# Kernel optimization log

Measured on AMD Instinct MI355X. Metric: run time of the kernel, lower is better.

The kernel has to match this reference:

```python
import jax, jax.numpy as jnp
import numpy as np

B = 16
H, D, DV = 8, 64, 64
MAX_SEQLEN = 1024
ALPHA = 1.0


def setup_inputs() -> dict:
    key = jax.random.key(0)
    lengths = np.array([512 + (b * 97) % 513 for b in range(B)], dtype=np.int32)
    offsets = np.concatenate([[0], np.cumsum(lengths)]).astype(np.int32)  # (B+1,)
    T = int(offsets[-1])  # 12137
    k1, k2, k3 = jax.random.split(key, 3)
    tq = jax.random.normal(k1, (T, H * D), dtype=jnp.float32)
    tk = jax.random.normal(k2, (T, H * D), dtype=jnp.float32)
    tv = jax.random.normal(k3, (T, H * DV), dtype=jnp.float32)
    num_candidates = jnp.full((B,), 32, dtype=jnp.int32)
    num_contextuals = jnp.full((B,), 8, dtype=jnp.int32)
    return {
        "tq": tq, "tk": tk, "tv": tv,
        "offsets": jnp.asarray(offsets),
        "max_seqlen": MAX_SEQLEN,
        "num_candidates": num_candidates,
        "num_contextuals": num_contextuals,
    }


def _valid_attn_mask(N, lengths, num_candidates, num_contextuals):
    # HSTU mask: causal within history, contextual tokens act as position 0
    # (attend/attended bidirectionally w.r.t. history), targets (candidates)
    # attend to all history + themselves only (target_group_size == 1).
    ids = jnp.arange(N, dtype=jnp.int32)[None, :]              # (1, N)
    c = num_contextuals[:, None]                                # (B, 1)
    ids_adj = jnp.maximum(ids - c + 1, 0)                       # (B, N)
    max_ids = (lengths - num_contextuals + 1 - num_candidates)[:, None]  # (B, 1)
    ids_adj = jnp.minimum(ids_adj, max_ids)                     # all targets share id == max_ids
    row = ids_adj[:, :, None]                                   # (B, N, 1)
    col = ids_adj[:, None, :]                                   # (B, 1, N)
    dist = row - col
    eye = jnp.eye(N, dtype=bool)[None]
    valid = eye | (dist > 0)                                    # causal + self
    # contextual rows (adjusted id 0) attend all history (but not targets)
    valid = valid | ((row == 0) & (col < max_ids[:, :, None]))
    # mask out padding
    pad = jnp.arange(N, dtype=jnp.int32)[None, :] < lengths[:, None]  # (B, N)
    valid = valid & pad[:, :, None] & pad[:, None, :]
    return valid


def reference(tq, tk, tv, offsets, max_seqlen, num_candidates, num_contextuals):
    T = tq.shape[0]
    Bb = offsets.shape[0] - 1
    N = max_seqlen
    lengths = offsets[1:] - offsets[:-1]                        # (B,)
    # jagged -> padded dense via scatter
    t = jnp.arange(T, dtype=jnp.int32)
    b_idx = jnp.searchsorted(offsets, t, side="right").astype(jnp.int32) - 1
    n_idx = t - offsets[b_idx]
    q = jnp.zeros((Bb, N, H, D), tq.dtype).at[b_idx, n_idx].set(tq.reshape(T, H, D))
    k = jnp.zeros((Bb, N, H, D), tk.dtype).at[b_idx, n_idx].set(tk.reshape(T, H, D))
    v = jnp.zeros((Bb, N, H, DV), tv.dtype).at[b_idx, n_idx].set(tv.reshape(T, H, DV))
    valid = _valid_attn_mask(N, lengths, num_candidates, num_contextuals)  # (B, N, N)
    qk = jnp.einsum("bnhd,bmhd->bhnm", q, k) * ALPHA
    # HSTU non-softmax attention: silu(scores) / max_seqlen, masked
    attn = (jax.nn.silu(qk) / N) * valid[:, None, :, :].astype(qk.dtype)
    out = jnp.einsum("bhnm,bmhd->bnhd", attn, v)                # (B, N, H, DV)
    # padded -> jagged gather
    return out[b_idx, n_idx].reshape(T, H * DV)
```

## Files before the change

kernel.cpp:

```cpp
#include <hip/hip_runtime.h>
#include <math.h>


#define HH      8
#define DDIM    64
#define QT      64
#define KT      64
#define STRIDE  512
#define NMAX    1024
#define NORD    16
#define TILE_HW 8192
#define NBLK    1024

typedef __attribute__((ext_vector_type(8))) short short8;
typedef __attribute__((ext_vector_type(4))) float f32x4;
typedef __attribute__((ext_vector_type(4))) uint  u32x4;

static __device__ __forceinline__ uint pk2(float a, float b) {
  uint r;
  asm("v_cvt_pk_bf16_f32 %0, %1, %2" : "=v"(r) : "v"(a), "v"(b));
  return r;
}

static __device__ __forceinline__ void dma16(const ushort* g, ushort* l) {
  __builtin_amdgcn_global_load_lds(
      (const __attribute__((address_space(1))) void*)g,
      (__attribute__((address_space(3))) void*)l, 16, 0, 0);
}

__global__ void build_tiles(const float* __restrict__ tk,
                            const float* __restrict__ tv,
                            ushort* __restrict__ tiles,
                            const int* __restrict__ offsets,
                            const int* __restrict__ pN) {
  const int mt = blockIdx.x, h = blockIdx.y, b = blockIdx.z;
  const int off = offsets[b];
  const int L   = offsets[b + 1] - off;
  if (mt * 64 >= L) return;
  const int tid = threadIdx.x;
  const float invN = 1.0f / (float)pN[0];

  __shared__ ushort tr[64][66];

  ushort* img = tiles + (size_t)((b * NORD + mt) * HH + h) * TILE_HW;
  const int row = tid >> 2;
  const int c0  = (tid & 3) * 16;
  const int m   = mt * 64 + row;
  const int sw  = (row & 7) << 3;

  {
    uint u[8];
    if (m < L) {
      const float* s = tk + (size_t)(off + m) * STRIDE + h * DDIM + c0;
      float4 a = *(const float4*)(s),      b4 = *(const float4*)(s + 4);
      float4 c4 = *(const float4*)(s + 8), d4 = *(const float4*)(s + 12);
      u[0] = pk2(a.x, a.y);   u[1] = pk2(a.z, a.w);
      u[2] = pk2(b4.x, b4.y); u[3] = pk2(b4.z, b4.w);
      u[4] = pk2(c4.x, c4.y); u[5] = pk2(c4.z, c4.w);
      u[6] = pk2(d4.x, d4.y); u[7] = pk2(d4.z, d4.w);
    } else {
#pragma unroll
      for (int j = 0; j < 8; ++j) u[j] = 0u;
    }
    *(uint4*)&img[row * 64 + (c0 ^ sw)]       = make_uint4(u[0], u[1], u[2], u[3]);
    *(uint4*)&img[row * 64 + ((c0 + 8) ^ sw)] = make_uint4(u[4], u[5], u[6], u[7]);
  }
  {
    uint u[8];
    if (m < L) {
      const float* s = tv + (size_t)(off + m) * STRIDE + h * DDIM + c0;
      float4 a = *(const float4*)(s),      b4 = *(const float4*)(s + 4);
      float4 c4 = *(const float4*)(s + 8), d4 = *(const float4*)(s + 12);
      u[0] = pk2(a.x * invN, a.y * invN);   u[1] = pk2(a.z * invN, a.w * invN);
      u[2] = pk2(b4.x * invN, b4.y * invN); u[3] = pk2(b4.z * invN, b4.w * invN);
      u[4] = pk2(c4.x * invN, c4.y * invN); u[5] = pk2(c4.z * invN, c4.w * invN);
      u[6] = pk2(d4.x * invN, d4.y * invN); u[7] = pk2(d4.z * invN, d4.w * invN);
    } else {
#pragma unroll
      for (int j = 0; j < 8; ++j) u[j] = 0u;
    }
#pragma unroll
    for (int j = 0; j < 8; ++j) *(uint*)&tr[row][c0 + 2 * j] = u[j];
  }
  __syncthreads();
  {
    const int dv = tid >> 2;
    const int tc = (tid & 3) * 16;
    uint u[8];
#pragma unroll
    for (int j = 0; j < 8; ++j)
      u[j] = (uint)tr[tc + 2 * j][dv] | ((uint)tr[tc + 2 * j + 1][dv] << 16);
    *(uint4*)&img[4096 + row * 64 + (c0 ^ sw)]       = make_uint4(u[0], u[1], u[2], u[3]);
    *(uint4*)&img[4096 + row * 64 + ((c0 + 8) ^ sw)] = make_uint4(u[4], u[5], u[6], u[7]);
  }
}

__global__ void zero_ctr(uint* ctr) { *ctr = 0u; }

__launch_bounds__(256, 4)
__global__ void hstu_s(const float* __restrict__ tq,
                       const ushort* __restrict__ tiles,
                       const int* __restrict__ offsets,
                       const int* __restrict__ ncand,
                       const int* __restrict__ nctx,
                       float* __restrict__ out, int Tm1, int Bb) {
  __shared__ ushort KV[2][TILE_HW];
  __shared__ ushort Ps[4 * 1024];

  const int tid  = threadIdx.x;
  const int w    = tid >> 6;
  const int lane = tid & 63;
  const int lo   = lane & 15;
  const int hi   = lane >> 4;

  int* scr = (int*)Ps;
  if (tid < 16)
    scr[tid] = (tid < Bb) ? (offsets[tid + 1] - offsets[tid] + QT - 1) / QT : 0;
  if (tid >= 16 && tid < 32) scr[tid] = -1;
  __syncthreads();
  if (tid < Bb) {
    const int nqb = scr[tid];
    int r = 0;
#pragma unroll
    for (int j = 0; j < 16; ++j) {
      int v = scr[j];
      r += (j < Bb) & ((v > nqb) | ((v == nqb) & (j < tid)));
    }
    if (r < Bb / 2) scr[16 + (r & 7)] = tid;
    else            scr[24 + ((Bb - 1 - r) & 7)] = tid;
  }
  __syncthreads();
  if (tid == 0) {
    const int g = blockIdx.x & 7, lb = blockIdx.x >> 3;
    const int gb0 = scr[16 + g], gb1 = scr[24 + g];
    const int q0 = (gb0 >= 0) ? scr[gb0] : -1;
    const int q1 = (gb1 >= 0) ? scr[gb1] : -1;
    const int i0 = lb >> 3,         h0 = lb & 7;
    const int i1 = (255 - lb) >> 3, h1 = (255 - lb) & 7;
    int cnt = 0, i = 0, e0 = -1, e1 = -1;
#pragma unroll
    for (int cst = 16; cst >= 1; --cst) {
#pragma unroll
      for (int s = 0; s < 2; ++s) {
        const int bb = (s == 0) ? gb0 : gb1;
        const int q  = (s == 0) ? q0 : q1;
        if (bb < 0) continue;
#pragma unroll
        for (int which = 0; which < 2; ++which) {
          int qt = -1;
          if (which == 0 && cst == q) qt = 0;
          if (which == 1 && cst >= 2 && cst <= q) qt = cst - 1;
          if (qt < 0) continue;
          const int enc = (bb << 7) | qt;
          if (i == i0) { e0 = enc | (h0 << 4); ++cnt; }
          if (i == i1) { e1 = enc | (h1 << 4); ++cnt; }
          ++i;
        }
      }
    }
    if (e0 < 0) { e0 = e1; e1 = -1; }
    scr[32] = e0; scr[33] = e1; scr[34] = cnt;
  }
  __syncthreads();
  const int e0  = scr[32];
  const int e1  = scr[33];
  const int cnt = scr[34];
  if (cnt == 0) return;

  ushort* Pw = &Ps[w * 1024];

  for (int it = 0; it < cnt; ++it) {
    const int e = (it == 0) ? e0 : e1;
    if (e < 0) return;
    const int b = (e >> 7) & 15, h = (e >> 4) & 7, qt = e & 15;
    const int off = offsets[b];
    const int L   = offsets[b + 1] - off;
    const int n0  = qt * QT;
    if (n0 >= L) continue;

    const int c = nctx[b];
    const int M = L - c + 1 - ncand[b];
    const int m_hi  = (n0 < c) ? L : min(n0 + QT, L);
    const int niter = (m_hi + KT - 1) / KT;

    const ushort* ibase = tiles + (size_t)(b * NORD * HH + h) * TILE_HW;

    __syncthreads();

    {
      const ushort* src = ibase + w * 2048 + lane * 8;
      ushort* dst = &KV[0][w * 2048];
#pragma unroll
      for (int i2 = 0; i2 < 4; ++i2) dma16(src + i2 * 512, dst + i2 * 512);
    }

    short8 qf[2];
    {
      int qr = min(off + n0 + w * 16 + lo, Tm1);
      const float* qp = tq + (size_t)qr * STRIDE + h * DDIM + hi * 8;
      float4 qa = *(const float4*)(qp);
      float4 qb = *(const float4*)(qp + 4);
      float4 qc = *(const float4*)(qp + 32);
      float4 qd = *(const float4*)(qp + 36);
      u32x4 v0 = {pk2(qa.x, qa.y), pk2(qa.z, qa.w), pk2(qb.x, qb.y), pk2(qb.z, qb.w)};
      u32x4 v1 = {pk2(qc.x, qc.y), pk2(qc.z, qc.w), pk2(qd.x, qd.y), pk2(qd.z, qd.w)};
      qf[0] = __builtin_bit_cast(short8, v0);
      qf[1] = __builtin_bit_cast(short8, v1);
    }

    const int  n   = n0 + w * 16 + lo;
    const int  an  = min(max(n - c + 1, 0), M);
    const int  thr = (an > 0 ? an : M) + c - 1;
    const bool nok = n < L;

    f32x4 oacc[4];
#pragma unroll
    for (int i2 = 0; i2 < 4; ++i2) oacc[i2] = (f32x4){0.f, 0.f, 0.f, 0.f};

    for (int t = 0; t < niter; ++t) {
      __syncthreads();

      if (t + 1 < niter) {
        const ushort* src = ibase + (size_t)(t + 1) * (HH * TILE_HW)
                            + w * 2048 + lane * 8;
        ushort* dst = &KV[(t + 1) & 1][w * 2048];
#pragma unroll
        for (int i2 = 0; i2 < 4; ++i2) dma16(src + i2 * 512, dst + i2 * 512);
      }

      const ushort* Kb = KV[t & 1];
      const ushort* Vb = Kb + 4096;
      const int m0 = t * KT;

#pragma unroll
      for (int kc = 0; kc < 4; ++kc) {
        const int krw = kc * 16 + lo;
        const int ksw = (krw & 7) << 3;
        short8 kf0 = *(const short8*)&Kb[krw * 64 + ((hi * 8) ^ ksw)];
        short8 kf1 = *(const short8*)&Kb[krw * 64 + ((32 + hi * 8) ^ ksw)];
        f32x4 s4 = (f32x4){0.f, 0.f, 0.f, 0.f};
        s4 = __builtin_amdgcn_mfma_f32_16x16x32_bf16(kf0, qf[0], s4, 0, 0, 0);
        s4 = __builtin_amdgcn_mfma_f32_16x16x32_bf16(kf1, qf[1], s4, 0, 0, 0);
        const int mb = m0 + kc * 16 + 4 * hi;
        float pp[4];
#pragma unroll
        for (int r = 0; r < 4; ++r) {
          const int mm = mb + r;
          const bool valid = nok & ((mm < thr) | (mm == n));
          float s = valid ? s4[r] : 0.f;
          pp[r] = s * __builtin_amdgcn_rcpf(1.f + __expf(-s));
        }
        const int col = kc * 16 + 4 * hi;
        *(uint2*)&Pw[lo * 64 + (col ^ ((lo & 7) << 3))] =
            make_uint2(pk2(pp[0], pp[1]), pk2(pp[2], pp[3]));
      }

#pragma unroll
      for (int mc = 0; mc < 2; ++mc) {
        short8 pf = *(const short8*)&Pw[lo * 64 + ((mc * 32 + hi * 8) ^ ((lo & 7) << 3))];
#pragma unroll
        for (int dvc = 0; dvc < 4; ++dvc) {
          const int vrow = dvc * 16 + lo;
          short8 vf = *(const short8*)&Vb[vrow * 64 + ((mc * 32 + hi * 8) ^ ((vrow & 7) << 3))];
          oacc[dvc] = __builtin_amdgcn_mfma_f32_16x16x32_bf16(pf, vf, oacc[dvc], 0, 0, 0);
        }
      }
    }

#pragma unroll
    for (int dvc = 0; dvc < 4; ++dvc) {
#pragma unroll
      for (int r = 0; r < 4; ++r) {
        int nn = n0 + w * 16 + hi * 4 + r;
        if (nn < L)
          out[(size_t)(off + nn) * STRIDE + h * DDIM + dvc * 16 + lo] = oacc[dvc][r];
      }
    }
  }
}

__launch_bounds__(256)
__global__ void hstu_fb(const float* __restrict__ tq,
                        const float* __restrict__ tk,
                        const float* __restrict__ tv,
                        const int* __restrict__ offsets,
                        const int* __restrict__ pN,
                        const int* __restrict__ ncand,
                        const int* __restrict__ nctx,
                        float* __restrict__ out,
                        uint* __restrict__ ctr,
                        int Tm1, int Bb) {
  const int bhc    = Bb * HH;
  const int nitems = NORD * bhc;

  __shared__ ushort Ks[KT * DDIM];
  __shared__ ushort Vt[DDIM * KT];
  __shared__ ushort Ps[4 * 1024];
  __shared__ int s_item;

  const int tid  = threadIdx.x;
  const int w    = tid >> 6;
  const int lane = tid & 63;
  const int lo   = lane & 15;
  const int hi   = lane >> 4;
  const float invN = 1.0f / (float)pN[0];
  ushort* Pw = &Ps[w * 1024];

  for (;;) {
    __syncthreads();
    if (tid == 0) s_item = (int)atomicAdd(ctr, 1u);
    __syncthreads();
    const int item = s_item;
    if (item >= nitems) return;
    const int ord = item / bhc;
    const int rem = item - ord * bhc;
    const int b = rem / HH, h = rem - b * HH;
    const int qt = (ord == 0) ? 0 : (NORD - ord);
    const int off = offsets[b];
    const int L   = offsets[b + 1] - off;
    const int n0  = qt * QT;
    if (n0 >= L) continue;

    const int c = nctx[b];
    const int M = L - c + 1 - ncand[b];
    const int m_hi  = (n0 < c) ? L : min(n0 + QT, L);
    const int niter = (m_hi + KT - 1) / KT;

    short8 qf[2];
    {
      int qr = min(off + n0 + w * 16 + lo, Tm1);
      const float* qp = tq + (size_t)qr * STRIDE + h * DDIM + hi * 8;
      float4 qa = *(const float4*)(qp);
      float4 qb = *(const float4*)(qp + 4);
      float4 qc = *(const float4*)(qp + 32);
      float4 qd = *(const float4*)(qp + 36);
      u32x4 v0 = {pk2(qa.x, qa.y), pk2(qa.z, qa.w), pk2(qb.x, qb.y), pk2(qb.z, qb.w)};
      u32x4 v1 = {pk2(qc.x, qc.y), pk2(qc.z, qc.w), pk2(qd.x, qd.y), pk2(qd.z, qd.w)};
      qf[0] = __builtin_bit_cast(short8, v0);
      qf[1] = __builtin_bit_cast(short8, v1);
    }

    const int  n   = n0 + w * 16 + lo;
    const int  an  = min(max(n - c + 1, 0), M);
    const int  thr = (an > 0 ? an : M) + c - 1;
    const bool nok = n < L;

    f32x4 oacc[4];
#pragma unroll
    for (int i = 0; i < 4; ++i) oacc[i] = (f32x4){0.f, 0.f, 0.f, 0.f};

    for (int t = 0; t < niter; ++t) {
      const int m0 = t * KT;
      __syncthreads();
#pragma unroll
      for (int jj = 0; jj < 4; ++jj) {
        int row = (tid >> 4) + jj * 16;
        int r2  = min(off + m0 + row, Tm1);
        float4 kv = *(const float4*)(tk + (size_t)r2 * STRIDE + h * DDIM + (tid & 15) * 4);
        uint2 pk;
        pk.x = pk2(kv.x, kv.y);
        pk.y = pk2(kv.z, kv.w);
        *(uint2*)&Ks[row * 64 + (((tid & 15) * 4) ^ ((row & 7) << 3))] = pk;
      }
      {
        uint bb[8];
#pragma unroll
        for (int j = 0; j < 8; ++j) {
          int ra = min(off + m0 + w * 16 + 2 * j,     Tm1);
          int rb = min(off + m0 + w * 16 + 2 * j + 1, Tm1);
          float va = tv[(size_t)ra * STRIDE + h * DDIM + lane];
          float vb = tv[(size_t)rb * STRIDE + h * DDIM + lane];
          bb[j] = pk2(va, vb);
        }
        int s = (lane & 7) << 3;
        *(uint4*)&Vt[lane * 64 + ((w * 16)     ^ s)] = make_uint4(bb[0], bb[1], bb[2], bb[3]);
        *(uint4*)&Vt[lane * 64 + ((w * 16 + 8) ^ s)] = make_uint4(bb[4], bb[5], bb[6], bb[7]);
      }
      __syncthreads();

#pragma unroll
      for (int kc = 0; kc < 4; ++kc) {
        const int krw = kc * 16 + lo;
        const int ksw = (krw & 7) << 3;
        short8 kf0 = *(const short8*)&Ks[krw * 64 + ((hi * 8) ^ ksw)];
        short8 kf1 = *(const short8*)&Ks[krw * 64 + ((32 + hi * 8) ^ ksw)];
        f32x4 s4 = (f32x4){0.f, 0.f, 0.f, 0.f};
        s4 = __builtin_amdgcn_mfma_f32_16x16x32_bf16(kf0, qf[0], s4, 0, 0, 0);
        s4 = __builtin_amdgcn_mfma_f32_16x16x32_bf16(kf1, qf[1], s4, 0, 0, 0);
        const int mb = m0 + kc * 16 + 4 * hi;
        float pp[4];
#pragma unroll
        for (int r = 0; r < 4; ++r) {
          const int mm = mb + r;
          const bool valid = nok & ((mm < thr) | (mm == n));
          float s = valid ? s4[r] : 0.f;
          pp[r] = s * invN * __builtin_amdgcn_rcpf(1.f + __expf(-s));
        }
        const int col = kc * 16 + 4 * hi;
        *(uint2*)&Pw[lo * 64 + (col ^ ((lo & 7) << 3))] =
            make_uint2(pk2(pp[0], pp[1]), pk2(pp[2], pp[3]));
      }

#pragma unroll
      for (int mc = 0; mc < 2; ++mc) {
        short8 pf = *(const short8*)&Pw[lo * 64 + ((mc * 32 + hi * 8) ^ ((lo & 7) << 3))];
#pragma unroll
        for (int dvc = 0; dvc < 4; ++dvc) {
          const int vrow = dvc * 16 + lo;
          short8 vf = *(const short8*)&Vt[vrow * 64 + ((mc * 32 + hi * 8) ^ ((vrow & 7) << 3))];
          oacc[dvc] = __builtin_amdgcn_mfma_f32_16x16x32_bf16(pf, vf, oacc[dvc], 0, 0, 0);
        }
      }
    }

#pragma unroll
    for (int dvc = 0; dvc < 4; ++dvc) {
#pragma unroll
      for (int r = 0; r < 4; ++r) {
        int nn = n0 + w * 16 + hi * 4 + r;
        if (nn < L)
          out[(size_t)(off + nn) * STRIDE + h * DDIM + dvc * 16 + lo] = oacc[dvc][r];
      }
    }
  }
}

extern "C" void kernel_launch(void* const* d_in, const int* in_sizes, int n_in,
                              void* d_out, int out_size, void* d_ws, size_t ws_size,
                              hipStream_t stream) {
  const float* tq      = (const float*)d_in[0];
  const float* tk      = (const float*)d_in[1];
  const float* tv      = (const float*)d_in[2];
  const int*   offsets = (const int*)d_in[3];
  const int*   pN      = (const int*)d_in[4];
  const int*   ncand   = (const int*)d_in[5];
  const int*   nctx    = (const int*)d_in[6];
  float*       out     = (float*)d_out;

  const int B = in_sizes[3] - 1;
  const int T = in_sizes[0] / STRIDE;

  uint*   ctr   = (uint*)d_ws;
  ushort* tiles = (ushort*)((char*)d_ws + 256);
  const size_t need = 256 + (size_t)B * NORD * HH * TILE_HW * sizeof(ushort);

  dim3 block(256);

  if (ws_size >= need && B <= 16) {
    dim3 tgrid(NORD, HH, B);
    build_tiles<<<tgrid, block, 0, stream>>>(tk, tv, tiles, offsets, pN);
    hstu_s<<<NBLK, block, 0, stream>>>(tq, tiles, offsets, ncand, nctx, out,
                                       T - 1, B);
  } else {
    zero_ctr<<<1, 1, 0, stream>>>(ctr);
    hstu_fb<<<NBLK, block, 0, stream>>>(tq, tk, tv, offsets, pN, ncand,
                                        nctx, out, ctr, T - 1, B);
  }
}
```

Measured before the change: 54.51 us.

## Double query tile height in hstu_s to reuse each K/V tile twice

Each block of the main kernel now handles two stacked 64-row query sub-tiles, which share every K/V tile loaded into LDS. This halves K/V traffic per query row and adds more MFMA work per synchronisation. The balanced two-item-per-block scheduler is replaced by a direct block-to-(batch, head, 128-row tile) mapping, with surplus blocks exiting early. In exchange the block uses more registers and LDS (occupancy hint drops from 4 to 3), causal masking wastes work on the diagonal for the larger tile, and load balance across blocks is coarser. A column index in the V-transpose pre-pass is also changed.

```diff
diff --git a/kernel.cpp b/kernel.cpp
--- a/kernel.cpp
+++ b/kernel.cpp
@@ -4,7 +4,7 @@
 
 #define HH      8
 #define DDIM    64
-#define QT      64
+#define QT2     128
 #define KT      64
 #define STRIDE  512
 #define NMAX    1024
@@ -90,14 +90,14 @@
 #pragma unroll
     for (int j = 0; j < 8; ++j)
       u[j] = (uint)tr[tc + 2 * j][dv] | ((uint)tr[tc + 2 * j + 1][dv] << 16);
-    *(uint4*)&img[4096 + row * 64 + (c0 ^ sw)]       = make_uint4(u[0], u[1], u[2], u[3]);
-    *(uint4*)&img[4096 + row * 64 + ((c0 + 8) ^ sw)] = make_uint4(u[4], u[5], u[6], u[7]);
+    *(uint4*)&img[4096 + row * 64 + (tc ^ sw)]       = make_uint4(u[0], u[1], u[2], u[3]);
+    *(uint4*)&img[4096 + row * 64 + ((tc + 8) ^ sw)] = make_uint4(u[4], u[5], u[6], u[7]);
   }
 }
 
 __global__ void zero_ctr(uint* ctr) { *ctr = 0u; }
 
-__launch_bounds__(256, 4)
+__launch_bounds__(256, 3)
 __global__ void hstu_s(const float* __restrict__ tq,
                        const ushort* __restrict__ tiles,
                        const int* __restrict__ offsets,
@@ -105,7 +105,7 @@
                        const int* __restrict__ nctx,
                        float* __restrict__ out, int Tm1, int Bb) {
   __shared__ ushort KV[2][TILE_HW];
-  __shared__ ushort Ps[4 * 1024];
+  __shared__ ushort Ps[8 * 1024];
 
   const int tid  = threadIdx.x;
   const int w    = tid >> 6;
@@ -115,7 +115,7 @@
 
   int* scr = (int*)Ps;
   if (tid < 16)
-    scr[tid] = (tid < Bb) ? (offsets[tid + 1] - offsets[tid] + QT - 1) / QT : 0;
+    scr[tid] = (tid < Bb) ? (offsets[tid + 1] - offsets[tid] + 63) / 64 : 0;
   if (tid >= 16 && tid < 32) scr[tid] = -1;
   __syncthreads();
   if (tid < Bb) {
@@ -130,151 +130,149 @@
     else            scr[24 + ((Bb - 1 - r) & 7)] = tid;
   }
   __syncthreads();
-  if (tid == 0) {
-    const int g = blockIdx.x & 7, lb = blockIdx.x >> 3;
-    const int gb0 = scr[16 + g], gb1 = scr[24 + g];
-    const int q0 = (gb0 >= 0) ? scr[gb0] : -1;
-    const int q1 = (gb1 >= 0) ? scr[gb1] : -1;
-    const int i0 = lb >> 3,         h0 = lb & 7;
-    const int i1 = (255 - lb) >> 3, h1 = (255 - lb) & 7;
-    int cnt = 0, i = 0, e0 = -1, e1 = -1;
-#pragma unroll
-    for (int cst = 16; cst >= 1; --cst) {
-#pragma unroll
-      for (int s = 0; s < 2; ++s) {
-        const int bb = (s == 0) ? gb0 : gb1;
-        const int q  = (s == 0) ? q0 : q1;
-        if (bb < 0) continue;
-#pragma unroll
-        for (int which = 0; which < 2; ++which) {
-          int qt = -1;
-          if (which == 0 && cst == q) qt = 0;
-          if (which == 1 && cst >= 2 && cst <= q) qt = cst - 1;
-          if (qt < 0) continue;
-          const int enc = (bb << 7) | qt;
-          if (i == i0) { e0 = enc | (h0 << 4); ++cnt; }
-          if (i == i1) { e1 = enc | (h1 << 4); ++cnt; }
-          ++i;
-        }
-      }
-    }
-    if (e0 < 0) { e0 = e1; e1 = -1; }
-    scr[32] = e0; scr[33] = e1; scr[34] = cnt;
-  }
-  __syncthreads();
-  const int e0  = scr[32];
-  const int e1  = scr[33];
-  const int cnt = scr[34];
-  if (cnt == 0) return;
-
-  ushort* Pw = &Ps[w * 1024];
-
-  for (int it = 0; it < cnt; ++it) {
-    const int e = (it == 0) ? e0 : e1;
-    if (e < 0) return;
-    const int b = (e >> 7) & 15, h = (e >> 4) & 7, qt = e & 15;
-    const int off = offsets[b];
-    const int L   = offsets[b + 1] - off;
-    const int n0  = qt * QT;
-    if (n0 >= L) continue;
-
-    const int c = nctx[b];
-    const int M = L - c + 1 - ncand[b];
-    const int m_hi  = (n0 < c) ? L : min(n0 + QT, L);
-    const int niter = (m_hi + KT - 1) / KT;
-
-    const ushort* ibase = tiles + (size_t)(b * NORD * HH + h) * TILE_HW;
-
+  const int g     = blockIdx.x & 7;
+  const int rest  = blockIdx.x >> 3;
+  const int h     = rest >> 4;
+  const int local = rest & 15;
+  const int b     = scr[16 + (local & 8) + g];
+  const int qt2   = local & 7;
+  if (b < 0) return;
+  const int nq  = scr[b];
+  const int nq2 = (nq + 1) >> 1;
+  if (qt2 >= nq2) return;
+
+  const int off = offsets[b];
+  const int L   = offsets[b + 1] - off;
+  const int n0  = qt2 * QT2;
+  const int c   = nctx[b];
+  const int M   = L - c + 1 - ncand[b];
+  const int m_hi  = (n0 < c) ? L : min(n0 + QT2, L);
+  const int niter = (m_hi + KT - 1) / KT;
+
+  const ushort* ibase = tiles + (size_t)(b * NORD * HH + h) * TILE_HW;
+
+  {
+    const ushort* src = ibase + w * 2048 + lane * 8;
+    ushort* dst = &KV[0][w * 2048];
+#pragma unroll
+    for (int i = 0; i < 4; ++i) dma16(src + i * 512, dst + i * 512);
+  }
+
+  short8 qfA[2], qfB[2];
+  {
+    int qr = min(off + n0 + w * 16 + lo, Tm1);
+    const float* qp = tq + (size_t)qr * STRIDE + h * DDIM + hi * 8;
+    float4 qa = *(const float4*)(qp);
+    float4 qb = *(const float4*)(qp + 4);
+    float4 qc = *(const float4*)(qp + 32);
+    float4 qd = *(const float4*)(qp + 36);
+    u32x4 v0 = {pk2(qa.x, qa.y), pk2(qa.z, qa.w), pk2(qb.x, qb.y), pk2(qb.z, qb.w)};
+    u32x4 v1 = {pk2(qc.x, qc.y), pk2(qc.z, qc.w), pk2(qd.x, qd.y), pk2(qd.z, qd.w)};
+    qfA[0] = __builtin_bit_cast(short8, v0);
+    qfA[1] = __builtin_bit_cast(short8, v1);
+  }
+  {
+    int qr = min(off + n0 + 64 + w * 16 + lo, Tm1);
+    const float* qp = tq + (size_t)qr * STRIDE + h * DDIM + hi * 8;
+    float4 qa = *(const float4*)(qp);
+    float4 qb = *(const float4*)(qp + 4);
+    float4 qc = *(const float4*)(qp + 32);
+    float4 qd = *(const float4*)(qp + 36);
+    u32x4 v0 = {pk2(qa.x, qa.y), pk2(qa.z, qa.w), pk2(qb.x, qb.y), pk2(qb.z, qb.w)};
+    u32x4 v1 = {pk2(qc.x, qc.y), pk2(qc.z, qc.w), pk2(qd.x, qd.y), pk2(qd.z, qd.w)};
+    qfB[0] = __builtin_bit_cast(short8, v0);
+    qfB[1] = __builtin_bit_cast(short8, v1);
+  }
+
+  const int  nA   = n0 + w * 16 + lo;
+  const int  anA  = min(max(nA - c + 1, 0), M);
+  const int  thrA = (anA > 0 ? anA : M) + c - 1;
+  const bool nokA = nA < L;
+  const int  nB   = nA + 64;
+  const int  anB  = min(max(nB - c + 1, 0), M);
+  const int  thrB = (anB > 0 ? anB : M) + c - 1;
+  const bool nokB = nB < L;
+
+  f32x4 oaccA[4], oaccB[4];
+#pragma unroll
+  for (int i = 0; i < 4; ++i) {
+    oaccA[i] = (f32x4){0.f, 0.f, 0.f, 0.f};
+    oaccB[i] = (f32x4){0.f, 0.f, 0.f, 0.f};
+  }
+
+  ushort* PwA = &Ps[w * 1024];
+  ushort* PwB = &Ps[(w + 4) * 1024];
+
+  for (int t = 0; t < niter; ++t) {
     __syncthreads();
 
-    {
-      const ushort* src = ibase + w * 2048 + lane * 8;
-      ushort* dst = &KV[0][w * 2048];
-#pragma unroll
-      for (int i2 = 0; i2 < 4; ++i2) dma16(src + i2 * 512, dst + i2 * 512);
-    }
-
-    short8 qf[2];
-    {
-      int qr = min(off + n0 + w * 16 + lo, Tm1);
-      const float* qp = tq + (size_t)qr * STRIDE + h * DDIM + hi * 8;
-      float4 qa = *(const float4*)(qp);
-      float4 qb = *(const float4*)(qp + 4);
-      float4 qc = *(const float4*)(qp + 32);
-      float4 qd = *(const float4*)(qp + 36);
-      u32x4 v0 = {pk2(qa.x, qa.y), pk2(qa.z, qa.w), pk2(qb.x, qb.y), pk2(qb.z, qb.w)};
-      u32x4 v1 = {pk2(qc.x, qc.y), pk2(qc.z, qc.w), pk2(qd.x, qd.y), pk2(qd.z, qd.w)};
-      qf[0] = __builtin_bit_cast(short8, v0);
-      qf[1] = __builtin_bit_cast(short8, v1);
-    }
-
-    const int  n   = n0 + w * 16 + lo;
-    const int  an  = min(max(n - c + 1, 0), M);
-    const int  thr = (an > 0 ? an : M) + c - 1;
-    const bool nok = n < L;
-
-    f32x4 oacc[4];
-#pragma unroll
-    for (int i2 = 0; i2 < 4; ++i2) oacc[i2] = (f32x4){0.f, 0.f, 0.f, 0.f};
-
-    for (int t = 0; t < niter; ++t) {
-      __syncthreads();
-
-      if (t + 1 < niter) {
-        const ushort* src = ibase + (size_t)(t + 1) * (HH * TILE_HW)
-                            + w * 2048 + lane * 8;
-        ushort* dst = &KV[(t + 1) & 1][w * 2048];
-#pragma unroll
-        for (int i2 = 0; i2 < 4; ++i2) dma16(src + i2 * 512, dst + i2 * 512);
-      }
-
-      const ushort* Kb = KV[t & 1];
-      const ushort* Vb = Kb + 4096;
-      const int m0 = t * KT;
-
-#pragma unroll
-      for (int kc = 0; kc < 4; ++kc) {
-        const int krw = kc * 16 + lo;
-        const int ksw = (krw & 7) << 3;
-        short8 kf0 = *(const short8*)&Kb[krw * 64 + ((hi * 8) ^ ksw)];
-        short8 kf1 = *(const short8*)&Kb[krw * 64 + ((32 + hi * 8) ^ ksw)];
-        f32x4 s4 = (f32x4){0.f, 0.f, 0.f, 0.f};
-        s4 = __builtin_amdgcn_mfma_f32_16x16x32_bf16(kf0, qf[0], s4, 0, 0, 0);
-        s4 = __builtin_amdgcn_mfma_f32_16x16x32_bf16(kf1, qf[1], s4, 0, 0, 0);
-        const int mb = m0 + kc * 16 + 4 * hi;
-        float pp[4];
-#pragma unroll
-        for (int r = 0; r < 4; ++r) {
-          const int mm = mb + r;
-          const bool valid = nok & ((mm < thr) | (mm == n));
-          float s = valid ? s4[r] : 0.f;
-          pp[r] = s * __builtin_amdgcn_rcpf(1.f + __expf(-s));
-        }
-        const int col = kc * 16 + 4 * hi;
-        *(uint2*)&Pw[lo * 64 + (col ^ ((lo & 7) << 3))] =
-            make_uint2(pk2(pp[0], pp[1]), pk2(pp[2], pp[3]));
-      }
-
-#pragma unroll
-      for (int mc = 0; mc < 2; ++mc) {
-        short8 pf = *(const short8*)&Pw[lo * 64 + ((mc * 32 + hi * 8) ^ ((lo & 7) << 3))];
-#pragma unroll
-        for (int dvc = 0; dvc < 4; ++dvc) {
-          const int vrow = dvc * 16 + lo;
-          short8 vf = *(const short8*)&Vb[vrow * 64 + ((mc * 32 + hi * 8) ^ ((vrow & 7) << 3))];
-          oacc[dvc] = __builtin_amdgcn_mfma_f32_16x16x32_bf16(pf, vf, oacc[dvc], 0, 0, 0);
-        }
-      }
-    }
-
-#pragma unroll
-    for (int dvc = 0; dvc < 4; ++dvc) {
+    if (t + 1 < niter) {
+      const ushort* src = ibase + (size_t)(t + 1) * (HH * TILE_HW)
+                          + w * 2048 + lane * 8;
+      ushort* dst = &KV[(t + 1) & 1][w * 2048];
+#pragma unroll
+      for (int i = 0; i < 4; ++i) dma16(src + i * 512, dst + i * 512);
+    }
+
+    const ushort* Kb = KV[t & 1];
+    const ushort* Vb = Kb + 4096;
+    const int m0 = t * KT;
+
+#pragma unroll
+    for (int kc = 0; kc < 4; ++kc) {
+      const int krw = kc * 16 + lo;
+      const int ksw = (krw & 7) << 3;
+      short8 kf0 = *(const short8*)&Kb[krw * 64 + ((hi * 8) ^ ksw)];
+      short8 kf1 = *(const short8*)&Kb[krw * 64 + ((32 + hi * 8) ^ ksw)];
+      f32x4 sa = (f32x4){0.f, 0.f, 0.f, 0.f};
+      sa = __builtin_amdgcn_mfma_f32_16x16x32_bf16(kf0, qfA[0], sa, 0, 0, 0);
+      sa = __builtin_amdgcn_mfma_f32_16x16x32_bf16(kf1, qfA[1], sa, 0, 0, 0);
+      f32x4 sb = (f32x4){0.f, 0.f, 0.f, 0.f};
+      sb = __builtin_amdgcn_mfma_f32_16x16x32_bf16(kf0, qfB[0], sb, 0, 0, 0);
+      sb = __builtin_amdgcn_mfma_f32_16x16x32_bf16(kf1, qfB[1], sb, 0, 0, 0);
+      const int mb = m0 + kc * 16 + 4 * hi;
+      float ppa[4], ppb[4];
 #pragma unroll
       for (int r = 0; r < 4; ++r) {
-        int nn = n0 + w * 16 + hi * 4 + r;
-        if (nn < L)
-          out[(size_t)(off + nn) * STRIDE + h * DDIM + dvc * 16 + lo] = oacc[dvc][r];
-      }
+        const int mm = mb + r;
+        const bool vA = nokA & ((mm < thrA) | (mm == nA));
+        float sAv = vA ? sa[r] : 0.f;
+        ppa[r] = sAv * __builtin_amdgcn_rcpf(1.f + __expf(-sAv));
+        const bool vB = nokB & ((mm < thrB) | (mm == nB));
+        float sBv = vB ? sb[r] : 0.f;
+        ppb[r] = sBv * __builtin_amdgcn_rcpf(1.f + __expf(-sBv));
+      }
+      const int col = kc * 16 + 4 * hi;
+      const int pso = lo * 64 + (col ^ ((lo & 7) << 3));
+      *(uint2*)&PwA[pso] = make_uint2(pk2(ppa[0], ppa[1]), pk2(ppa[2], ppa[3]));
+      *(uint2*)&PwB[pso] = make_uint2(pk2(ppb[0], ppb[1]), pk2(ppb[2], ppb[3]));
+    }
+
+#pragma unroll
+    for (int mc = 0; mc < 2; ++mc) {
+      const int pro = lo * 64 + ((mc * 32 + hi * 8) ^ ((lo & 7) << 3));
+      short8 pfA = *(const short8*)&PwA[pro];
+      short8 pfB = *(const short8*)&PwB[pro];
+#pragma unroll
+      for (int dvc = 0; dvc < 4; ++dvc) {
+        const int vrow = dvc * 16 + lo;
+        short8 vf = *(const short8*)&Vb[vrow * 64 + ((mc * 32 + hi * 8) ^ ((vrow & 7) << 3))];
+        oaccA[dvc] = __builtin_amdgcn_mfma_f32_16x16x32_bf16(pfA, vf, oaccA[dvc], 0, 0, 0);
+        oaccB[dvc] = __builtin_amdgcn_mfma_f32_16x16x32_bf16(pfB, vf, oaccB[dvc], 0, 0, 0);
+      }
+    }
+  }
+
+#pragma unroll
+  for (int dvc = 0; dvc < 4; ++dvc) {
+#pragma unroll
+    for (int r = 0; r < 4; ++r) {
+      int nn = n0 + w * 16 + hi * 4 + r;
+      if (nn < L)
+        out[(size_t)(off + nn) * STRIDE + h * DDIM + dvc * 16 + lo] = oaccA[dvc][r];
+      int nn2 = nn + 64;
+      if (nn2 < L)
+        out[(size_t)(off + nn2) * STRIDE + h * DDIM + dvc * 16 + lo] = oaccB[dvc][r];
     }
   }
 }
@@ -318,12 +316,12 @@
     const int qt = (ord == 0) ? 0 : (NORD - ord);
     const int off = offsets[b];
     const int L   = offsets[b + 1] - off;
-    const int n0  = qt * QT;
+    const int n0  = qt * 64;
     if (n0 >= L) continue;
 
     const int c = nctx[b];
     const int M = L - c + 1 - ncand[b];
-    const int m_hi  = (n0 < c) ? L : min(n0 + QT, L);
+    const int m_hi  = (n0 < c) ? L : min(n0 + 64, L);
     const int niter = (m_hi + KT - 1) / KT;
 
     short8 qf[2];
```

After: 77.17 us. 41.6% more time.
